# Kernel optimization log

Hardware: AMD Instinct MI355X
Metric: run time of the kernel (lower is better)

## Reference

```python
import jax, jax.numpy as jnp
import numpy as np

B, L, C = 4, 2048, 1024
H = 16
D = C // H  # head_dim = 64


def _rope(t, cos, sin):
    # t: [B, H, L, D]; cos/sin: [L, D//2] broadcast to [1, 1, L, D//2]
    te = t[..., ::2]
    to = t[..., 1::2]
    c = cos[None, None]
    s = sin[None, None]
    re = te * c - to * s
    ro = te * s + to * c
    # interleave even/odd back: [..., D//2, 2] -> [..., D]
    return jnp.stack([re, ro], axis=-1).reshape(t.shape)


def setup_inputs() -> dict:
    key = jax.random.key(0)
    ks = jax.random.split(key, 5)
    x = jax.random.normal(ks[0], (B, L, C), dtype=jnp.float32)
    # rotary phases: theta_i = 10000^(-2i/D), angles = pos * theta
    inv_freq = 1.0 / (10000.0 ** (np.arange(0, D, 2, dtype=np.float32) / D))
    ang = np.arange(L, dtype=np.float32)[:, None] * inv_freq[None, :]  # [L, D//2]
    cos = jnp.asarray(np.cos(ang))
    sin = jnp.asarray(np.sin(ang))
    w_qkv = jax.random.normal(ks[1], (3 * C, C), dtype=jnp.float32) * (C ** -0.5)
    w_proj = jax.random.normal(ks[2], (C, C), dtype=jnp.float32) * (C ** -0.5)
    b_proj = jnp.zeros((C,), dtype=jnp.float32)
    return {"x": x, "cos": cos, "sin": sin, "w_qkv": w_qkv, "w_proj": w_proj, "b_proj": b_proj}


def reference(x, cos, sin, w_qkv, w_proj, b_proj):
    Bx, Lx, Cx = x.shape
    # QKV projection (torch Linear: y = x @ W.T), then split heads
    qkv = jnp.einsum("blc,fc->blf", x, w_qkv)  # [B, L, 3C]
    qkv = qkv.reshape(Bx, Lx, 3, H, D).transpose(2, 0, 3, 1, 4)  # [3, B, H, L, D]
    q, k, v = qkv[0], qkv[1], qkv[2]
    q = _rope(q, cos, sin)
    k = _rope(k, cos, sin)
    # scaled dot-product attention, non-causal
    scale = D ** -0.5
    scores = jnp.einsum("bhqd,bhkd->bhqk", q, k) * scale
    attn = jax.nn.softmax(scores, axis=-1)
    o = jnp.einsum("bhqk,bhkd->bhqd", attn, v)  # [B, H, L, D]
    o = o.transpose(0, 2, 1, 3).reshape(Bx, Lx, Cx)
    return jnp.einsum("blc,fc->blf", o, w_proj) + b_proj
```

## Files before the change

### kernel.cpp

```cpp
#include <hip/hip_runtime.h>
#include <hip/hip_bf16.h>
#include <cstdint>


typedef unsigned short u16;
typedef __attribute__((ext_vector_type(8))) short bf16x8;
typedef __attribute__((ext_vector_type(4))) float f32x4;

#define GLD16(g, l)                                                            \
  __builtin_amdgcn_global_load_lds(                                            \
      (const __attribute__((address_space(1))) void*)(g),                      \
      (__attribute__((address_space(3))) void*)(l), 16, 0, 0)

static __device__ __forceinline__ u16 f32_bf16(float f) {
  union { float f; unsigned u; } v; v.f = f;
  unsigned r = v.u + 0x7FFFu + ((v.u >> 16) & 1u);
  return (u16)(r >> 16);
}
static __device__ __forceinline__ float bf16_f32(u16 h) {
  union { unsigned u; float f; } v; v.u = ((unsigned)h) << 16;
  return v.f;
}
static __device__ __forceinline__ unsigned pack_rne(float a, float b) {
  union { float f; unsigned u; } x, y; x.f = a; y.f = b;
  unsigned ua = x.u + 0x7FFFu + ((x.u >> 16) & 1u);
  unsigned ub = y.u + 0x7FFFu + ((y.u >> 16) & 1u);
  return (ua >> 16) | (ub & 0xFFFF0000u);
}
static __device__ __forceinline__ unsigned pack_bf16_hw(float a, float b) {
  float2 t; t.x = a; t.y = b;
  __hip_bfloat162 h = __float22bfloat162_rn(t);
  union { __hip_bfloat162 h; unsigned u; } c; c.h = h;
  return c.u;
}

__global__ __launch_bounds__(256) void convert_all(
    const void* __restrict__ x, const void* __restrict__ wq,
    const void* __restrict__ wp, const void* __restrict__ cs,
    const void* __restrict__ sn, const void* __restrict__ bs,
    u16* __restrict__ xb, u16* __restrict__ wqb, u16* __restrict__ wpb,
    u16* __restrict__ cb, u16* __restrict__ sb, u16* __restrict__ bb) {
  const unsigned f32mode = (((const unsigned*)cs)[0] == 0x3F800000u);
  int blk = blockIdx.x;
  const void* src; u16* dst; int i0, n4;
  if (blk < 8192)       { src = x;  dst = xb;  i0 = blk;         n4 = 2097152; }
  else if (blk < 11264) { src = wq; dst = wqb; i0 = blk - 8192;  n4 = 786432; }
  else if (blk < 12288) { src = wp; dst = wpb; i0 = blk - 11264; n4 = 262144; }
  else if (blk < 12352) { src = cs; dst = cb;  i0 = blk - 12288; n4 = 16384; }
  else if (blk < 12416) { src = sn; dst = sb;  i0 = blk - 12352; n4 = 16384; }
  else                  { src = bs; dst = bb;  i0 = blk - 12416; n4 = 256; }
  int i = i0 * 256 + threadIdx.x;
  if (i >= n4) return;
  if (f32mode) {
    float4 v = ((const float4*)src)[i];
    uint2 o;
    o.x = pack_rne(v.x, v.y);
    o.y = pack_rne(v.z, v.w);
    ((uint2*)dst)[i] = o;
  } else {
    ((uint2*)dst)[i] = ((const uint2*)src)[i];
  }
}

static __device__ __forceinline__ void gemm_mainloop(
    const u16* __restrict__ A, const u16* __restrict__ Bm, int K,
    int m0, int n0, u16* As, u16* Bs, f32x4 acc[4][4]) {
  const int tid  = threadIdx.x;
  const int lane = tid & 63;
  const int wave = tid >> 6;
  const int n16  = lane & 15;
  const int quad = lane >> 4;
  const int wm = (wave >> 1) * 64;
  const int wn = (wave & 1) * 64;
  const u16* ag = A  + (size_t)(m0 + wave * 16 + (lane >> 2)) * K + (lane & 3) * 8;
  const u16* bg = Bm + (size_t)(n0 + wave * 16 + (lane >> 2)) * K + (lane & 3) * 8;
  u16* al = As + wave * (16 * 32);
  u16* bl = Bs + wave * (16 * 32);
  for (int kt = 0; kt < K; kt += 32) {
    GLD16(ag + kt, al);
    GLD16(ag + (size_t)64 * K + kt, al + 64 * 32);
    GLD16(bg + kt, bl);
    GLD16(bg + (size_t)64 * K + kt, bl + 64 * 32);
    __syncthreads();
    bf16x8 af[4], bf[4];
#pragma unroll
    for (int i = 0; i < 4; i++)
      af[i] = *(const bf16x8*)(As + (wm + i * 16 + n16) * 32 + quad * 8);
#pragma unroll
    for (int j = 0; j < 4; j++)
      bf[j] = *(const bf16x8*)(Bs + (wn + j * 16 + n16) * 32 + quad * 8);
#pragma unroll
    for (int i = 0; i < 4; i++)
#pragma unroll
      for (int j = 0; j < 4; j++)
        acc[i][j] = __builtin_amdgcn_mfma_f32_16x16x32_bf16(af[i], bf[j], acc[i][j], 0, 0, 0);
    __syncthreads();
  }
}

__global__ __launch_bounds__(256) void gemm_qkv(
    const u16* __restrict__ x, const u16* __restrict__ w,
    u16* __restrict__ q_ws, u16* __restrict__ k_ws, u16* __restrict__ vt_ws) {
  __shared__ u16 As[128 * 32];
  __shared__ u16 Bs[128 * 32];
  f32x4 acc[4][4];
#pragma unroll
  for (int i = 0; i < 4; i++)
#pragma unroll
    for (int j = 0; j < 4; j++) acc[i][j] = (f32x4){0.f, 0.f, 0.f, 0.f};
  const int m0 = blockIdx.y * 128;
  const int n0 = blockIdx.x * 128;
  gemm_mainloop(x, w, 1024, m0, n0, As, Bs, acc);
  const int lane = threadIdx.x & 63, wave = threadIdx.x >> 6;
  const int n16 = lane & 15, quad = lane >> 4;
  const int wm = (wave >> 1) * 64, wn = (wave & 1) * 64;
#pragma unroll
  for (int i = 0; i < 4; i++)
#pragma unroll
    for (int j = 0; j < 4; j++) {
      int f = n0 + wn + j * 16 + n16;
      int which = f >> 10;
      int rem = f & 1023;
      int h = rem >> 6, d = rem & 63;
      int l0 = m0 + wm + i * 16 + quad * 4;
      int b = l0 >> 11, l = l0 & 2047;
      if (which == 2) {
        uint2 o;
        o.x = pack_rne(acc[i][j][0], acc[i][j][1]);
        o.y = pack_rne(acc[i][j][2], acc[i][j][3]);
        size_t idx = (((size_t)b * 16 + h) * 64 + d) * 2048 + l;
        *(uint2*)(vt_ws + idx) = o;
      } else {
        u16* dst = (which == 0) ? q_ws : k_ws;
        size_t base = (((size_t)b * 16 + h) * 2048 + l) * 64 + d;
#pragma unroll
        for (int r = 0; r < 4; r++)
          dst[base + (size_t)r * 64] = f32_bf16(acc[i][j][r]);
      }
    }
}

#define NP_ROPE 4194304
__global__ __launch_bounds__(256) void rope_qk(
    u16* __restrict__ q, u16* __restrict__ k,
    const u16* __restrict__ cosp, const u16* __restrict__ sinp) {
  int idx = blockIdx.x * 256 + threadIdx.x;
  u16* t = (idx < NP_ROPE) ? q : k;
  int p = (idx < NP_ROPE) ? idx : idx - NP_ROPE;
  int l = (p >> 5) & 2047;
  int i = p & 31;
  unsigned v = ((unsigned*)t)[p];
  float te = bf16_f32((u16)(v & 0xFFFFu));
  float to = bf16_f32((u16)(v >> 16));
  float c = bf16_f32(cosp[l * 32 + i]);
  float s = bf16_f32(sinp[l * 32 + i]);
  ((unsigned*)t)[p] = pack_rne(te * c - to * s, te * s + to * c);
}

__global__ __launch_bounds__(256, 4) void flash_attn(
    const u16* __restrict__ q_ws, const u16* __restrict__ k_ws,
    const u16* __restrict__ vt_ws, u16* __restrict__ o_ws) {
  __shared__ u16 Ks[64 * 64];
  __shared__ u16 Vs[64 * 64];
  __shared__ u16 Pa[4 * 32 * 72];
  const int bh = blockIdx.y;
  const int q0 = blockIdx.x * 128;
  const int b = bh >> 4, h = bh & 15;
  const int tid = threadIdx.x, lane = tid & 63, wave = tid >> 6;
  const int n16 = lane & 15, quad = lane >> 4;
  const int x7 = n16 & 7;
  const size_t hoff = (size_t)bh * (2048 * 64);

  bf16x8 qf[2][2];
#pragma unroll
  for (int qb = 0; qb < 2; qb++) {
    const u16* qrow = q_ws + hoff + (size_t)(q0 + wave * 32 + qb * 16 + n16) * 64;
    qf[qb][0] = *(const bf16x8*)(qrow + quad * 8);
    qf[qb][1] = *(const bf16x8*)(qrow + 32 + quad * 8);
  }

  f32x4 oacc[2][4];
#pragma unroll
  for (int qb = 0; qb < 2; qb++)
#pragma unroll
    for (int s = 0; s < 4; s++) oacc[qb][s] = (f32x4){0.f, 0.f, 0.f, 0.f};
  f32x4 lq[2];
  lq[0] = (f32x4){0.f, 0.f, 0.f, 0.f};
  lq[1] = (f32x4){0.f, 0.f, 0.f, 0.f};

  const int srow = wave * 8 + (lane >> 3);
  const int sw = (lane & 7) ^ ((lane >> 3) & 7);
  const u16* kg = k_ws + hoff + (size_t)srow * 64 + sw * 8;
  const u16* vg = vt_ws + hoff + (size_t)srow * 2048 + sw * 8;
  u16* kl = Ks + wave * 8 * 64;
  u16* vl = Vs + wave * 8 * 64;
  u16* const pw = Pa + wave * (32 * 72);

  for (int kt = 0; kt < 2048; kt += 64) {
    GLD16(kg + (size_t)kt * 64, kl);
    GLD16(kg + (size_t)kt * 64 + 32 * 64, kl + 32 * 64);
    GLD16(vg + kt, vl);
    GLD16(vg + kt + (size_t)32 * 2048, vl + 32 * 64);
    __syncthreads();

#pragma unroll
    for (int sub = 0; sub < 4; sub++) {
      const u16* krow = Ks + (sub * 16 + n16) * 64;
      bf16x8 kf0 = *(const bf16x8*)(krow + (quad ^ x7) * 8);
      bf16x8 kf1 = *(const bf16x8*)(krow + ((quad + 4) ^ x7) * 8);
#pragma unroll
      for (int qb = 0; qb < 2; qb++) {
        f32x4 z = (f32x4){0.f, 0.f, 0.f, 0.f};
        z = __builtin_amdgcn_mfma_f32_16x16x32_bf16(kf0, qf[qb][0], z, 0, 0, 0);
        z = __builtin_amdgcn_mfma_f32_16x16x32_bf16(kf1, qf[qb][1], z, 0, 0, 0);
        f32x4 p;
#pragma unroll
        for (int r = 0; r < 4; r++) p[r] = __expf(z[r] * 0.125f);
        lq[qb] += p;
        uint2 o;
        o.x = pack_bf16_hw(p[0], p[1]);
        o.y = pack_bf16_hw(p[2], p[3]);
        *(uint2*)(pw + (qb * 16 + n16) * 72 + quad * 4 + sub * 16) = o;
      }
    }

    bf16x8 pf[2][2];
#pragma unroll
    for (int qb = 0; qb < 2; qb++) {
      const u16* prow = pw + (qb * 16 + n16) * 72;
      pf[qb][0] = *(const bf16x8*)(prow + quad * 8);
      pf[qb][1] = *(const bf16x8*)(prow + 32 + quad * 8);
    }
#pragma unroll
    for (int sd = 0; sd < 4; sd++) {
      const u16* vrow = Vs + (sd * 16 + n16) * 64;
      bf16x8 vf0 = *(const bf16x8*)(vrow + (quad ^ x7) * 8);
      bf16x8 vf1 = *(const bf16x8*)(vrow + ((quad + 4) ^ x7) * 8);
#pragma unroll
      for (int qb = 0; qb < 2; qb++) {
        oacc[qb][sd] = __builtin_amdgcn_mfma_f32_16x16x32_bf16(pf[qb][0], vf0, oacc[qb][sd], 0, 0, 0);
        oacc[qb][sd] = __builtin_amdgcn_mfma_f32_16x16x32_bf16(pf[qb][1], vf1, oacc[qb][sd], 0, 0, 0);
      }
    }
    __syncthreads();
  }

#pragma unroll
  for (int qb = 0; qb < 2; qb++) {
    float l = lq[qb][0] + lq[qb][1] + lq[qb][2] + lq[qb][3];
    l += __shfl_xor(l, 16, 64);
    l += __shfl_xor(l, 32, 64);
    float linv = 1.0f / l;
#pragma unroll
    for (int r = 0; r < 4; r++) {
      float lr = __shfl(linv, quad * 4 + r, 64);
      int row = q0 + wave * 32 + qb * 16 + quad * 4 + r;
      size_t base = ((size_t)b * 2048 + row) * 1024 + h * 64;
#pragma unroll
      for (int sd = 0; sd < 4; sd++)
        o_ws[base + sd * 16 + n16] = f32_bf16(oacc[qb][sd][r] * lr);
    }
  }
}

__global__ __launch_bounds__(256) void gemm_proj(
    const u16* __restrict__ o, const u16* __restrict__ w,
    const u16* __restrict__ bias, float* __restrict__ out) {
  __shared__ u16 As[128 * 32];
  __shared__ u16 Bs[128 * 32];
  f32x4 acc[4][4];
#pragma unroll
  for (int i = 0; i < 4; i++)
#pragma unroll
    for (int j = 0; j < 4; j++) acc[i][j] = (f32x4){0.f, 0.f, 0.f, 0.f};
  const int m0 = blockIdx.y * 128;
  const int n0 = blockIdx.x * 128;
  gemm_mainloop(o, w, 1024, m0, n0, As, Bs, acc);
  const int lane = threadIdx.x & 63, wave = threadIdx.x >> 6;
  const int n16 = lane & 15, quad = lane >> 4;
  const int wm = (wave >> 1) * 64, wn = (wave & 1) * 64;
#pragma unroll
  for (int i = 0; i < 4; i++)
#pragma unroll
    for (int j = 0; j < 4; j++) {
      int f = n0 + wn + j * 16 + n16;
      float bf = bf16_f32(bias[f]);
#pragma unroll
      for (int r = 0; r < 4; r++) {
        int m = m0 + wm + i * 16 + quad * 4 + r;
        out[(size_t)m * 1024 + f] = acc[i][j][r] + bf;
      }
    }
}

extern "C" void kernel_launch(void* const* d_in, const int* in_sizes, int n_in,
                              void* d_out, int out_size, void* d_ws, size_t ws_size,
                              hipStream_t stream) {
  float* out = (float*)d_out;

  u16* ws = (u16*)d_ws;
  u16* xb     = ws;
  u16* wqkvb  = ws + 8388608;
  u16* wprojb = ws + 11534336;
  u16* cosb   = ws + 12582912;
  u16* sinb   = ws + 12648448;
  u16* biasb  = ws + 12713984;
  u16* qb     = ws + 12715008;
  u16* kb     = ws + 21103616;
  u16* vtb    = ws + 29492224;
  u16* ob     = xb;

  convert_all<<<12417, 256, 0, stream>>>(
      d_in[0], d_in[3], d_in[4], d_in[1], d_in[2], d_in[5],
      xb, wqkvb, wprojb, cosb, sinb, biasb);

  gemm_qkv<<<dim3(24, 64), 256, 0, stream>>>(xb, wqkvb, qb, kb, vtb);
  rope_qk<<<32768, 256, 0, stream>>>(qb, kb, cosb, sinb);
  flash_attn<<<dim3(16, 64), 256, 0, stream>>>(qb, kb, vtb, ob);
  gemm_proj<<<dim3(8, 64), 256, 0, stream>>>(ob, wprojb, biasb, out);
}
```

Measured before the change: 320.3 us.

## Double-buffer K/V tiles, widen attention blocks, fold softmax scale into Q

The flash-attention kernel now double-buffers K and V tiles in shared memory, so the next tile's global-to-LDS load is issued while the current tile is computed. This drops one barrier per iteration. Each wave now handles 64 query rows instead of 32, which doubles reuse of every K/V tile, and the grid is flattened to 512 blocks with the head index varying fastest. The softmax scale times log2(e) is folded into Q during RoPE so the inner loop can use a raw exp2. The cost is higher register and LDS use, with occupancy lowered to 2 blocks per CU, and fewer total blocks.

```diff
diff --git a/kernel.cpp b/kernel.cpp
--- a/kernel.cpp
+++ b/kernel.cpp
@@ -145,8 +145,10 @@
     u16* __restrict__ q, u16* __restrict__ k,
     const u16* __restrict__ cosp, const u16* __restrict__ sinp) {
   int idx = blockIdx.x * 256 + threadIdx.x;
-  u16* t = (idx < NP_ROPE) ? q : k;
-  int p = (idx < NP_ROPE) ? idx : idx - NP_ROPE;
+  bool isq = (idx < NP_ROPE);
+  u16* t = isq ? q : k;
+  float sc = isq ? 0.18033688011112042f : 1.0f;
+  int p = isq ? idx : idx - NP_ROPE;
   int l = (p >> 5) & 2047;
   int i = p & 31;
   unsigned v = ((unsigned*)t)[p];
@@ -154,68 +156,79 @@
   float to = bf16_f32((u16)(v >> 16));
   float c = bf16_f32(cosp[l * 32 + i]);
   float s = bf16_f32(sinp[l * 32 + i]);
-  ((unsigned*)t)[p] = pack_rne(te * c - to * s, te * s + to * c);
-}
-
-__global__ __launch_bounds__(256, 4) void flash_attn(
+  ((unsigned*)t)[p] = pack_rne((te * c - to * s) * sc, (te * s + to * c) * sc);
+}
+
+__global__ __launch_bounds__(256, 2) void flash_attn(
     const u16* __restrict__ q_ws, const u16* __restrict__ k_ws,
     const u16* __restrict__ vt_ws, u16* __restrict__ o_ws) {
-  __shared__ u16 Ks[64 * 64];
-  __shared__ u16 Vs[64 * 64];
-  __shared__ u16 Pa[4 * 32 * 72];
-  const int bh = blockIdx.y;
-  const int q0 = blockIdx.x * 128;
+  __shared__ u16 Ks[2][64 * 64];
+  __shared__ u16 Vs[2][64 * 64];
+  __shared__ u16 Pa[4 * 64 * 72];
+  const int bh = blockIdx.x & 63;
+  const int q0 = (blockIdx.x >> 6) * 256;
   const int b = bh >> 4, h = bh & 15;
   const int tid = threadIdx.x, lane = tid & 63, wave = tid >> 6;
   const int n16 = lane & 15, quad = lane >> 4;
   const int x7 = n16 & 7;
   const size_t hoff = (size_t)bh * (2048 * 64);
 
-  bf16x8 qf[2][2];
-#pragma unroll
-  for (int qb = 0; qb < 2; qb++) {
-    const u16* qrow = q_ws + hoff + (size_t)(q0 + wave * 32 + qb * 16 + n16) * 64;
+  bf16x8 qf[4][2];
+#pragma unroll
+  for (int qb = 0; qb < 4; qb++) {
+    const u16* qrow = q_ws + hoff + (size_t)(q0 + wave * 64 + qb * 16 + n16) * 64;
     qf[qb][0] = *(const bf16x8*)(qrow + quad * 8);
     qf[qb][1] = *(const bf16x8*)(qrow + 32 + quad * 8);
   }
 
-  f32x4 oacc[2][4];
-#pragma unroll
-  for (int qb = 0; qb < 2; qb++)
+  f32x4 oacc[4][4];
+  f32x4 lq[4];
+#pragma unroll
+  for (int qb = 0; qb < 4; qb++) {
+    lq[qb] = (f32x4){0.f, 0.f, 0.f, 0.f};
 #pragma unroll
     for (int s = 0; s < 4; s++) oacc[qb][s] = (f32x4){0.f, 0.f, 0.f, 0.f};
-  f32x4 lq[2];
-  lq[0] = (f32x4){0.f, 0.f, 0.f, 0.f};
-  lq[1] = (f32x4){0.f, 0.f, 0.f, 0.f};
+  }
 
   const int srow = wave * 8 + (lane >> 3);
   const int sw = (lane & 7) ^ ((lane >> 3) & 7);
   const u16* kg = k_ws + hoff + (size_t)srow * 64 + sw * 8;
   const u16* vg = vt_ws + hoff + (size_t)srow * 2048 + sw * 8;
-  u16* kl = Ks + wave * 8 * 64;
-  u16* vl = Vs + wave * 8 * 64;
-  u16* const pw = Pa + wave * (32 * 72);
+  const int loff = wave * 8 * 64;
+  u16* const pw = Pa + wave * (64 * 72);
+
+  GLD16(kg, &Ks[0][loff]);
+  GLD16(kg + 32 * 64, &Ks[0][loff + 32 * 64]);
+  GLD16(vg, &Vs[0][loff]);
+  GLD16(vg + (size_t)32 * 2048, &Vs[0][loff + 32 * 64]);
 
   for (int kt = 0; kt < 2048; kt += 64) {
-    GLD16(kg + (size_t)kt * 64, kl);
-    GLD16(kg + (size_t)kt * 64 + 32 * 64, kl + 32 * 64);
-    GLD16(vg + kt, vl);
-    GLD16(vg + kt + (size_t)32 * 2048, vl + 32 * 64);
+    const int buf = (kt >> 6) & 1;
     __syncthreads();
+    if (kt + 64 < 2048) {
+      const u16* kgn = kg + (size_t)(kt + 64) * 64;
+      const u16* vgn = vg + (kt + 64);
+      GLD16(kgn, &Ks[buf ^ 1][loff]);
+      GLD16(kgn + 32 * 64, &Ks[buf ^ 1][loff + 32 * 64]);
+      GLD16(vgn, &Vs[buf ^ 1][loff]);
+      GLD16(vgn + (size_t)32 * 2048, &Vs[buf ^ 1][loff + 32 * 64]);
+    }
+    const u16* ks = Ks[buf];
+    const u16* vs = Vs[buf];
 
 #pragma unroll
     for (int sub = 0; sub < 4; sub++) {
-      const u16* krow = Ks + (sub * 16 + n16) * 64;
+      const u16* krow = ks + (sub * 16 + n16) * 64;
       bf16x8 kf0 = *(const bf16x8*)(krow + (quad ^ x7) * 8);
       bf16x8 kf1 = *(const bf16x8*)(krow + ((quad + 4) ^ x7) * 8);
 #pragma unroll
-      for (int qb = 0; qb < 2; qb++) {
+      for (int qb = 0; qb < 4; qb++) {
         f32x4 z = (f32x4){0.f, 0.f, 0.f, 0.f};
         z = __builtin_amdgcn_mfma_f32_16x16x32_bf16(kf0, qf[qb][0], z, 0, 0, 0);
         z = __builtin_amdgcn_mfma_f32_16x16x32_bf16(kf1, qf[qb][1], z, 0, 0, 0);
         f32x4 p;
 #pragma unroll
-        for (int r = 0; r < 4; r++) p[r] = __expf(z[r] * 0.125f);
+        for (int r = 0; r < 4; r++) p[r] = __builtin_amdgcn_exp2f(z[r]);
         lq[qb] += p;
         uint2 o;
         o.x = pack_bf16_hw(p[0], p[1]);
@@ -224,29 +237,28 @@
       }
     }
 
-    bf16x8 pf[2][2];
-#pragma unroll
-    for (int qb = 0; qb < 2; qb++) {
+    bf16x8 pf[4][2];
+#pragma unroll
+    for (int qb = 0; qb < 4; qb++) {
       const u16* prow = pw + (qb * 16 + n16) * 72;
       pf[qb][0] = *(const bf16x8*)(prow + quad * 8);
       pf[qb][1] = *(const bf16x8*)(prow + 32 + quad * 8);
     }
 #pragma unroll
     for (int sd = 0; sd < 4; sd++) {
-      const u16* vrow = Vs + (sd * 16 + n16) * 64;
+      const u16* vrow = vs + (sd * 16 + n16) * 64;
       bf16x8 vf0 = *(const bf16x8*)(vrow + (quad ^ x7) * 8);
       bf16x8 vf1 = *(const bf16x8*)(vrow + ((quad + 4) ^ x7) * 8);
 #pragma unroll
-      for (int qb = 0; qb < 2; qb++) {
+      for (int qb = 0; qb < 4; qb++) {
         oacc[qb][sd] = __builtin_amdgcn_mfma_f32_16x16x32_bf16(pf[qb][0], vf0, oacc[qb][sd], 0, 0, 0);
         oacc[qb][sd] = __builtin_amdgcn_mfma_f32_16x16x32_bf16(pf[qb][1], vf1, oacc[qb][sd], 0, 0, 0);
       }
     }
-    __syncthreads();
-  }
-
-#pragma unroll
-  for (int qb = 0; qb < 2; qb++) {
+  }
+
+#pragma unroll
+  for (int qb = 0; qb < 4; qb++) {
     float l = lq[qb][0] + lq[qb][1] + lq[qb][2] + lq[qb][3];
     l += __shfl_xor(l, 16, 64);
     l += __shfl_xor(l, 32, 64);
@@ -254,7 +266,7 @@
 #pragma unroll
     for (int r = 0; r < 4; r++) {
       float lr = __shfl(linv, quad * 4 + r, 64);
-      int row = q0 + wave * 32 + qb * 16 + quad * 4 + r;
+      int row = q0 + wave * 64 + qb * 16 + quad * 4 + r;
       size_t base = ((size_t)b * 2048 + row) * 1024 + h * 64;
 #pragma unroll
       for (int sd = 0; sd < 4; sd++)
@@ -316,6 +328,6 @@
 
   gemm_qkv<<<dim3(24, 64), 256, 0, stream>>>(xb, wqkvb, qb, kb, vtb);
   rope_qk<<<32768, 256, 0, stream>>>(qb, kb, cosb, sinb);
-  flash_attn<<<dim3(16, 64), 256, 0, stream>>>(qb, kb, vtb, ob);
+  flash_attn<<<512, 256, 0, stream>>>(qb, kb, vtb, ob);
   gemm_proj<<<dim3(8, 64), 256, 0, stream>>>(ob, wprojb, biasb, out);
 }
```

Result: faster. 286.5 us (-10.6%).
